# Performance work log

Measured on AMD Instinct MI355X. Metric: run time of the kernel, lower is better.

Reference implementation:

```python
import jax, jax.numpy as jnp
import numpy as np

D_MODEL = 1024
N_HEADS = 16
D_HEAD = 64


def setup_inputs() -> dict:
    key = jax.random.key(0)
    ks = jax.random.split(key, 9)
    B, T = 2, 2048
    s_in = 1.0 / np.sqrt(D_MODEL)
    s_o = 1.0 / np.sqrt(N_HEADS * D_HEAD)
    return {
        "x": jax.random.normal(ks[0], (B, T, D_MODEL), dtype=jnp.float32),
        "wq": jax.random.normal(ks[1], (D_MODEL, N_HEADS * D_HEAD), dtype=jnp.float32) * s_in,
        "bq": jax.random.normal(ks[2], (N_HEADS * D_HEAD,), dtype=jnp.float32) * 0.01,
        "wk": jax.random.normal(ks[3], (D_MODEL, N_HEADS * D_HEAD), dtype=jnp.float32) * s_in,
        "bk": jax.random.normal(ks[4], (N_HEADS * D_HEAD,), dtype=jnp.float32) * 0.01,
        "wv": jax.random.normal(ks[5], (D_MODEL, N_HEADS * D_HEAD), dtype=jnp.float32) * s_in,
        "bv": jax.random.normal(ks[6], (N_HEADS * D_HEAD,), dtype=jnp.float32) * 0.01,
        "wo": jax.random.normal(ks[7], (N_HEADS * D_HEAD, D_MODEL), dtype=jnp.float32) * s_o,
        "bo": jax.random.normal(ks[8], (D_MODEL,), dtype=jnp.float32) * 0.01,
    }


def reference(x, wq, bq, wk, bk, wv, bv, wo, bo):
    B, T, _ = x.shape
    H, Dh = N_HEADS, D_HEAD
    # projections -> [B, H, T, Dh]
    q = (x @ wq + bq).reshape(B, T, H, Dh).transpose(0, 2, 1, 3)
    k = (x @ wk + bk).reshape(B, T, H, Dh).transpose(0, 2, 1, 3)
    v = (x @ wv + bv).reshape(B, T, H, Dh).transpose(0, 2, 1, 3)
    scale = 1.0 / np.sqrt(Dh).astype(np.float32)
    attn = jnp.einsum("bhqd,bhkd->bhqk", q, k) * scale  # [B,H,T,T]
    causal = jnp.tril(jnp.ones((T, T), dtype=bool))
    attn = jnp.where(causal, attn, jnp.float32(-jnp.inf))
    attn = jax.nn.softmax(attn, axis=-1)
    out = jnp.einsum("bhqk,bhkd->bhqd", attn, v)  # [B,H,T,Dh]
    out = out.transpose(0, 2, 1, 3).reshape(B, T, H * Dh)
    return out @ wo + bo
```

## Files before the change

### kernel.cpp

```cpp
#include <hip/hip_runtime.h>
#include <math.h>

#define D_MODEL 1024
#define N_HEADS 16
#define D_HEAD  64
#define B_SZ    2
#define T_SEQ   2048
#define WN_ELEMS (1024u * 1024u)

typedef short bf16x8 __attribute__((ext_vector_type(8)));
typedef short bf16x4 __attribute__((ext_vector_type(4)));
typedef float f32x4  __attribute__((ext_vector_type(4)));
typedef unsigned short us4 __attribute__((ext_vector_type(4)));

__device__ __forceinline__ unsigned short f2bf(float f) {
  union { float f; unsigned u; } v; v.f = f;
  unsigned r = v.u + 0x7FFFu + ((v.u >> 16) & 1u);
  return (unsigned short)(r >> 16);
}
__device__ __forceinline__ float bf2f(unsigned short s) {
  union { unsigned u; float f; } v; v.u = ((unsigned)s) << 16;
  return v.f;
}
__device__ __forceinline__ unsigned pack2_rtz(float lo, float hi) {
  union { float f; unsigned u; } a, b; a.f = hi; b.f = lo;
  return __builtin_amdgcn_perm(a.u, b.u, 0x07060302u);
}

__device__ __forceinline__ void async_copy16(const unsigned short* g, unsigned short* l) {
  __builtin_amdgcn_global_load_lds(
      (__attribute__((address_space(1))) void*)(g),
      (__attribute__((address_space(3))) void*)(l), 16, 0, 0);
}

__device__ __forceinline__ size_t widx(int n, int k) {
  const int fb = n >> 5, mi = (n >> 4) & 1, lr = n & 15;
  const int kt = k >> 6, hf = (k >> 5) & 1, quad = (k >> 3) & 3, e = k & 7;
  return ((size_t)(fb * 16 + kt) * 4 + (mi * 2 + hf)) * 512 + (quad * 16 + lr) * 8 + e;
}

__device__ __forceinline__ unsigned short* opart_ptr(
    unsigned short* wtd, unsigned short* xbd, int p) {
  const size_t off = (size_t)p * 2048;
  const size_t RA  = (size_t)3 * 1024 * 1024;
  return (off < RA) ? (wtd + off) : (xbd + (off - RA));
}

__global__ __launch_bounds__(256) void conv_all(
    const float* __restrict__ x,
    const float* __restrict__ wq, const float* __restrict__ wk,
    const float* __restrict__ wv, const float* __restrict__ wo,
    unsigned short* __restrict__ wt, unsigned short* __restrict__ xb)
{
  const int z = blockIdx.z;
  if (z < 4) {
    const float* W = (z == 0) ? wq : (z == 1) ? wk : (z == 2) ? wv : wo;
    unsigned short* O = wt + (size_t)z * WN_ELEMS;
    __shared__ float t[32][33];
    const int tx = threadIdx.x & 31, ty = threadIdx.x >> 5;
    const int kb = blockIdx.x * 32, nb = blockIdx.y * 32;
    #pragma unroll
    for (int i = 0; i < 4; i++)
      t[ty + i * 8][tx] = W[(size_t)(kb + ty + i * 8) * D_MODEL + nb + tx];
    __syncthreads();
    #pragma unroll
    for (int i = 0; i < 4; i++)
      O[widx(nb + ty + i * 8, kb + tx)] = f2bf(t[tx][ty + i * 8]);
  } else {
    const int row = (z - 4) * 1024 + blockIdx.y * 32 + (threadIdx.x >> 3);
    const int col = blockIdx.x * 32 + (threadIdx.x & 7) * 4;
    float4 v = *(const float4*)&x[(size_t)row * D_MODEL + col];
    us4 o = { f2bf(v.x), f2bf(v.y), f2bf(v.z), f2bf(v.w) };
    *(us4*)&xb[(size_t)row * D_MODEL + col] = o;
  }
}

#define BKg 64
#define NTg (D_MODEL / BKg)
#define QSCALE 0.180336879f

__global__ __launch_bounds__(256) void qkv_gemm(
    const unsigned short* __restrict__ A, const unsigned short* __restrict__ Bt,
    const float* __restrict__ bq, const float* __restrict__ bk,
    const float* __restrict__ bv, unsigned short* __restrict__ qkv,
    unsigned short* __restrict__ vT)
{
  __shared__ unsigned short As[2][128 * BKg];

  const int tid  = threadIdx.x;
  const int wv   = tid >> 6;
  const int lane = tid & 63;
  const int lr   = lane & 15;
  const int quad = lane >> 4;
  const int wm   = wv >> 1;
  const int wn   = wv & 1;
  const int row0 = blockIdx.x * 128;
  const int col0 = blockIdx.y * 64;
  const int K = D_MODEL;

  const int mid = col0 >> 10;
  const float* bias = (mid == 0) ? bq : (mid == 1) ? bk : bv;

  f32x4 acc[8];
  #pragma unroll
  for (int i = 0; i < 8; i++) acc[i] = (f32x4){0.f, 0.f, 0.f, 0.f};

  auto stageA = [&](int buf, int k0) {
    #pragma unroll
    for (int it = 0; it < 4; it++) {
      const int gg = wv * 256 + it * 64 + lane;
      const int r  = gg >> 3;
      const int gc = ((gg & 7) ^ (r & 7)) * 8;
      async_copy16(A + (size_t)(row0 + r) * K + k0 + gc,
                   &As[buf][(size_t)(wv * 256 + it * 64) * 8]);
    }
  };

  const int wsel = (mid == 2) ? wn : wm;
  const int fb   = ((col0 & 1023) >> 5) + wsel;
  const unsigned short* Wp =
      Bt + (size_t)mid * WN_ELEMS + (size_t)fb * (16 * 2048) + lane * 8;

  auto loadW = [&](int kt, bf16x8 (&W)[2][2]) {
    #pragma unroll
    for (int mi = 0; mi < 2; mi++)
      #pragma unroll
      for (int hf = 0; hf < 2; hf++)
        W[mi][hf] = *(const bf16x8*)&Wp[((size_t)kt * 4 + mi * 2 + hf) * 512];
  };

  const int xrow = (mid == 2) ? wm : wn;

  bf16x8 Wc[2][2], Wn[2][2];
  loadW(0, Wc);
  stageA(0, 0);
  int cur = 0;

  auto kstep = [&](int t, bf16x8 (&Wuse)[2][2], bf16x8 (&Wpre)[2][2]) {
    __syncthreads();

    bf16x8 xF[4][2];
    #pragma unroll
    for (int hf = 0; hf < 2; hf++) {
      const int kc = ((hf * 4 + quad) ^ (lr & 7)) * 8;
      #pragma unroll
      for (int ni = 0; ni < 4; ni++)
        xF[ni][hf] = *(const bf16x8*)&As[cur][(xrow * 64 + ni * 16 + lr) * BKg + kc];
    }

    if (t + 1 < NTg) {
      stageA(cur ^ 1, (t + 1) * BKg);
      loadW(t + 1, Wpre);
    }

    if (mid == 2) {
      #pragma unroll
      for (int hf = 0; hf < 2; hf++)
        #pragma unroll
        for (int mi = 0; mi < 4; mi++)
          #pragma unroll
          for (int ni = 0; ni < 2; ni++)
            acc[mi * 2 + ni] = __builtin_amdgcn_mfma_f32_16x16x32_bf16(
                xF[mi][hf], Wuse[ni][hf], acc[mi * 2 + ni], 0, 0, 0);
    } else {
      #pragma unroll
      for (int hf = 0; hf < 2; hf++)
        #pragma unroll
        for (int mi = 0; mi < 2; mi++)
          #pragma unroll
          for (int ni = 0; ni < 4; ni++)
            acc[mi * 4 + ni] = __builtin_amdgcn_mfma_f32_16x16x32_bf16(
                Wuse[mi][hf], xF[ni][hf], acc[mi * 4 + ni], 0, 0, 0);
    }
    cur ^= 1;
  };

  #pragma unroll 1
  for (int t = 0; t < NTg; t += 2) {
    kstep(t,     Wc, Wn);
    kstep(t + 1, Wn, Wc);
  }

  if (mid == 2) {
    #pragma unroll
    for (int ni = 0; ni < 2; ni++) {
      const int nn = (col0 & 1023) + wn * 32 + ni * 16 + lr;
      const float bv_ = bias[nn];
      const int h = nn >> 6, d = nn & 63;
      #pragma unroll
      for (int mi = 0; mi < 4; mi++) {
        const int t0_ = row0 + wm * 64 + mi * 16 + quad * 4;
        const int b = t0_ >> 11, tl = t0_ & 2047;
        us4 o;
        #pragma unroll
        for (int i = 0; i < 4; i++) o[i] = f2bf(acc[mi * 2 + ni][i] + bv_);
        *(us4*)&vT[((size_t)(b * N_HEADS + h) * D_HEAD + d) * T_SEQ + tl] = o;
      }
    }
  } else {
    unsigned short* dst = qkv + (size_t)mid * (4096u * 1024u);
    const float qs = (mid == 0) ? QSCALE : 1.0f;
    #pragma unroll
    for (int ni = 0; ni < 4; ni++) {
      const int t = row0 + wn * 64 + ni * 16 + lr;
      const int b = t >> 11, tl = t & 2047;
      #pragma unroll
      for (int mi = 0; mi < 2; mi++) {
        const int f = (col0 & 1023) + wm * 32 + mi * 16 + quad * 4;
        const int h = f >> 6, d = f & 63;
        const float4 b4 = *(const float4*)&bias[f];
        us4 o;
        o[0] = f2bf((acc[mi * 4 + ni][0] + b4.x) * qs);
        o[1] = f2bf((acc[mi * 4 + ni][1] + b4.y) * qs);
        o[2] = f2bf((acc[mi * 4 + ni][2] + b4.z) * qs);
        o[3] = f2bf((acc[mi * 4 + ni][3] + b4.w) * qs);
        *(us4*)&dst[((size_t)(b * N_HEADS + h) * T_SEQ + tl) * D_HEAD + d] = o;
      }
    }
  }
}

__global__ __launch_bounds__(256) void mfma_gemm(
    const unsigned short* __restrict__ A, const unsigned short* __restrict__ Bt,
    const float* __restrict__ bias, float* __restrict__ C,
    int M, int N, int K)
{
  __shared__ unsigned short As[2][128 * BKg];

  const int tid  = threadIdx.x;
  const int wv   = tid >> 6;
  const int lane = tid & 63;
  const int lr   = lane & 15;
  const int quad = lane >> 4;
  const int wm   = wv >> 1;
  const int wn   = wv & 1;
  const int row0 = blockIdx.x * 128;
  const int col0 = blockIdx.y * 64;

  f32x4 acc[4][2];
  #pragma unroll
  for (int mi = 0; mi < 4; mi++)
    #pragma unroll
    for (int ni = 0; ni < 2; ni++) acc[mi][ni] = (f32x4){0.f, 0.f, 0.f, 0.f};

  auto stageA = [&](int buf, int k0) {
    #pragma unroll
    for (int it = 0; it < 4; it++) {
      const int gg = wv * 256 + it * 64 + lane;
      const int r  = gg >> 3;
      const int gc = ((gg & 7) ^ (r & 7)) * 8;
      async_copy16(A + (size_t)(row0 + r) * K + k0 + gc,
                   &As[buf][(size_t)(wv * 256 + it * 64) * 8]);
    }
  };

  const int fb = (col0 >> 5) + wn;
  const unsigned short* Wp = Bt + (size_t)fb * (16 * 2048) + lane * 8;
  auto loadW = [&](int kt, bf16x8 (&W)[2][2]) {
    #pragma unroll
    for (int ni = 0; ni < 2; ni++)
      #pragma unroll
      for (int hf = 0; hf < 2; hf++)
        W[ni][hf] = *(const bf16x8*)&Wp[((size_t)kt * 4 + ni * 2 + hf) * 512];
  };

  const int NT = K / BKg;
  bf16x8 Wc[2][2], Wn[2][2];
  loadW(0, Wc);
  stageA(0, 0);
  int cur = 0;

  auto kstep = [&](int t, bf16x8 (&Wuse)[2][2], bf16x8 (&Wpre)[2][2]) {
    __syncthreads();

    bf16x8 aF[4][2];
    #pragma unroll
    for (int hf = 0; hf < 2; hf++) {
      const int kc = ((hf * 4 + quad) ^ (lr & 7)) * 8;
      #pragma unroll
      for (int mi = 0; mi < 4; mi++)
        aF[mi][hf] = *(const bf16x8*)&As[cur][(wm * 64 + mi * 16 + lr) * BKg + kc];
    }

    if (t + 1 < NT) {
      stageA(cur ^ 1, (t + 1) * BKg);
      loadW(t + 1, Wpre);
    }

    #pragma unroll
    for (int hf = 0; hf < 2; hf++)
      #pragma unroll
      for (int mi = 0; mi < 4; mi++)
        #pragma unroll
        for (int ni = 0; ni < 2; ni++)
          acc[mi][ni] = __builtin_amdgcn_mfma_f32_16x16x32_bf16(
              aF[mi][hf], Wuse[ni][hf], acc[mi][ni], 0, 0, 0);
    cur ^= 1;
  };

  #pragma unroll 1
  for (int t = 0; t < NT; t += 2) {
    kstep(t,     Wc, Wn);
    kstep(t + 1, Wn, Wc);
  }

  #pragma unroll
  for (int ni = 0; ni < 2; ni++) {
    const int n = col0 + wn * 32 + ni * 16 + lr;
    const float bv = bias[n];
    #pragma unroll
    for (int mi = 0; mi < 4; mi++) {
      #pragma unroll
      for (int i = 0; i < 4; i++) {
        const int m = row0 + wm * 64 + mi * 16 + quad * 4 + i;
        C[(size_t)m * N + n] = acc[mi][ni][i] + bv;
      }
    }
  }
}

__global__ __launch_bounds__(256) void flash_part(
    const unsigned short* __restrict__ Q, const unsigned short* __restrict__ K,
    const unsigned short* __restrict__ Vt, unsigned short* __restrict__ Out,
    unsigned short* __restrict__ OpA, unsigned short* __restrict__ OpB,
    float* __restrict__ Lpart)
{
  const int bh = blockIdx.x;
  const int y  = blockIdx.y;
  int g, md;
  if (y < 28) { g = 15 - (y >> 1); md = 1 + (y & 1); }
  else        { g = 29 - y; md = 0; }

  const int b  = bh >> 4;
  const int h  = bh & 15;

  const unsigned short* Qb = Q  + (size_t)bh * T_SEQ * D_HEAD;
  const unsigned short* Kb = K  + (size_t)bh * T_SEQ * D_HEAD;
  const unsigned short* Vb = Vt + (size_t)bh * D_HEAD * T_SEQ;

  __shared__ __align__(16) unsigned short Ks[2][64 * 64];
  __shared__ __align__(16) unsigned short Vs[2][64 * 64];

  const int tid  = threadIdx.x;
  const int wv4  = tid >> 6;
  const int lane = tid & 63;
  const int lr   = lane & 15;
  const int quad = lane >> 4;

  const int qg      = 4 * g + wv4;
  const int q0      = qg * 32;
  const int my_full = 2 * g + 1 + (wv4 >> 1);
  const int tstart  = (md == 2) ? (g + 1) : 0;
  const int bend    = (md == 1) ? (g + 1) : (2 * g + 2);
  const int my_end  = (md == 1) ? (g + 1) : my_full;

  const int cbase = (tid & ~63);
  const int rr = tid >> 3;
  const int gcf = ((tid & 7) ^ (rr & 7)) * 8;
  const unsigned short* kp0 = Kb + (size_t)rr * D_HEAD + gcf;
  const unsigned short* vp0 = Vb + (size_t)rr * T_SEQ + gcf;

  auto stage = [&](int buf, int tile) {
    const unsigned short* kt = kp0 + (size_t)tile * (64 * D_HEAD);
    const unsigned short* vt = vp0 + (size_t)tile * 64;
    async_copy16(kt,                    &Ks[buf][(size_t)cbase * 8]);
    async_copy16(kt + 32 * D_HEAD,      &Ks[buf][(size_t)(256 + cbase) * 8]);
    async_copy16(vt,                    &Vs[buf][(size_t)cbase * 8]);
    async_copy16(vt + (size_t)32 * T_SEQ, &Vs[buf][(size_t)(256 + cbase) * 8]);
  };

  bf16x8 bQ[2][2];
  #pragma unroll
  for (int qb = 0; qb < 2; qb++)
    #pragma unroll
    for (int kh = 0; kh < 2; kh++)
      bQ[qb][kh] = *(const bf16x8*)&Qb[(size_t)(q0 + qb * 16 + lr) * D_HEAD + kh * 32 + quad * 8];

  f32x4 oacc[2][4];
  #pragma unroll
  for (int qb = 0; qb < 2; qb++)
    #pragma unroll
    for (int dt = 0; dt < 4; dt++) oacc[qb][dt] = (f32x4){0.f, 0.f, 0.f, 0.f};
  f32x4 lacc[2] = {(f32x4){0.f, 0.f, 0.f, 0.f}, (f32x4){0.f, 0.f, 0.f, 0.f}};

  const bf16x4 vONE = {(short)0x3F80, (short)0x3F80, (short)0x3F80, (short)0x3F80};

  int cur = 0;
  stage(0, tstart);

  for (int j = tstart; j < bend; j++) {
    __syncthreads();
    const bool act = (j < my_end);
    const unsigned short* KsB = &Ks[cur][0];
    const unsigned short* VsB = &Vs[cur][0];
    const int kv0 = j * 64;

    bf16x8 aK[4][2];
    bf16x4 aV[4][4];
    if (act) {
      #pragma unroll
      for (int nt = 0; nt < 4; nt++) {
        const int row = nt * 16 + lr;
        #pragma unroll
        for (int kh = 0; kh < 2; kh++) {
          const int sc = (kh * 4 + quad) ^ (row & 7);
          aK[nt][kh] = *(const bf16x8*)&KsB[row * 64 + sc * 8];
        }
      }
      #pragma unroll
      for (int dt = 0; dt < 4; dt++) {
        const int row = dt * 16 + lr;
        #pragma unroll
        for (int ks = 0; ks < 4; ks++) {
          const int sc = (ks * 2 + (quad >> 1)) ^ (row & 7);
          aV[dt][ks] = *(const bf16x4*)&VsB[row * 64 + sc * 8 + (quad & 1) * 4];
        }
      }
    }

    if (j + 1 < bend) stage(cur ^ 1, j + 1);

    if (act) {
      f32x4 sacc[2][4];
      __builtin_amdgcn_s_setprio(1);
      #pragma unroll
      for (int nt = 0; nt < 4; nt++) {
        #pragma unroll
        for (int qb = 0; qb < 2; qb++) {
          f32x4 c = (f32x4){0.f, 0.f, 0.f, 0.f};
          c = __builtin_amdgcn_mfma_f32_16x16x32_bf16(aK[nt][0], bQ[qb][0], c, 0, 0, 0);
          c = __builtin_amdgcn_mfma_f32_16x16x32_bf16(aK[nt][1], bQ[qb][1], c, 0, 0, 0);
          sacc[qb][nt] = c;
        }
      }
      __builtin_amdgcn_s_setprio(0);

      const bool diag = (j == my_full - 1);
      bf16x4 bP[2][4];
      #pragma unroll
      for (int qb = 0; qb < 2; qb++) {
        if (diag) {
          const int qcol = q0 + qb * 16 + lr;
          #pragma unroll
          for (int nt = 0; nt < 4; nt++)
            #pragma unroll
            for (int i = 0; i < 4; i++)
              if (kv0 + nt * 16 + quad * 4 + i > qcol) sacc[qb][nt][i] = -INFINITY;
        }
        #pragma unroll
        for (int nt = 0; nt < 4; nt++) {
          float p[4];
          #pragma unroll
          for (int i = 0; i < 4; i++)
            p[i] = __builtin_amdgcn_exp2f(sacc[qb][nt][i]);
          union { unsigned u[2]; bf16x4 v; } pk;
          pk.u[0] = pack2_rtz(p[0], p[1]);
          pk.u[1] = pack2_rtz(p[2], p[3]);
          bP[qb][nt] = pk.v;
        }
      }

      __builtin_amdgcn_s_setprio(1);
      #pragma unroll
      for (int ks = 0; ks < 4; ks++) {
        #pragma unroll
        for (int qb = 0; qb < 2; qb++) {
          lacc[qb] = __builtin_amdgcn_mfma_f32_16x16x16bf16_1k(
              vONE, bP[qb][ks], lacc[qb], 0, 0, 0);
          #pragma unroll
          for (int dt = 0; dt < 4; dt++)
            oacc[qb][dt] = __builtin_amdgcn_mfma_f32_16x16x16bf16_1k(
                aV[dt][ks], bP[qb][ks], oacc[qb][dt], 0, 0, 0);
        }
      }
      __builtin_amdgcn_s_setprio(0);
    }
    cur ^= 1;
  }

  float l_i[2] = {lacc[0][0], lacc[1][0]};

  if (md == 0) {
    #pragma unroll
    for (int qb = 0; qb < 2; qb++) {
      const float invl = __builtin_amdgcn_rcpf(l_i[qb]);
      const size_t orow = (size_t)(b * T_SEQ + q0 + qb * 16 + lr) * D_MODEL + h * D_HEAD;
      #pragma unroll
      for (int dt = 0; dt < 4; dt++) {
        us4 o;
        #pragma unroll
        for (int i = 0; i < 4; i++) o[i] = f2bf(oacc[qb][dt][i] * invl);
        *(us4*)&Out[orow + dt * 16 + quad * 4] = o;
      }
    }
  } else {
    const int s = md - 1;
    const int p = (bh * 56 + (qg - 8)) * 2 + s;
    unsigned short* Op = opart_ptr(OpA, OpB, p);
    if (quad == 0) {
      Lpart[(p * 2 + 0) * 16 + lr] = l_i[0];
      Lpart[(p * 2 + 1) * 16 + lr] = l_i[1];
    }
    #pragma unroll
    for (int qb = 0; qb < 2; qb++) {
      #pragma unroll
      for (int dt = 0; dt < 4; dt++) {
        us4 o;
        #pragma unroll
        for (int i = 0; i < 4; i++) o[i] = f2bf(oacc[qb][dt][i]);
        *(us4*)&Op[(size_t)(((qb * 4 + dt) * 64) + lane) * 4] = o;
      }
    }
  }
}

__global__ __launch_bounds__(64) void flash_reduce(
    unsigned short* __restrict__ OpA, unsigned short* __restrict__ OpB,
    const float* __restrict__ Lpart, unsigned short* __restrict__ Out)
{
  const int bh  = blockIdx.x;
  const int qgr = blockIdx.y;
  const int q0  = (8 + qgr) * 32;
  const int b   = bh >> 4;
  const int h   = bh & 15;
  const int lane = threadIdx.x;
  const int lr   = lane & 15;
  const int quad = lane >> 4;

  const int item = bh * 56 + qgr;
  const int p0 = item * 2, p1 = item * 2 + 1;
  const unsigned short* O0 = opart_ptr(OpA, OpB, p0);
  const unsigned short* O1 = opart_ptr(OpA, OpB, p1);

  #pragma unroll
  for (int qb = 0; qb < 2; qb++) {
    const float l0 = Lpart[(p0 * 2 + qb) * 16 + lr];
    const float l1 = Lpart[(p1 * 2 + qb) * 16 + lr];
    const float invL = __builtin_amdgcn_rcpf(l0 + l1);
    const size_t orow = (size_t)(b * T_SEQ + q0 + qb * 16 + lr) * D_MODEL + h * D_HEAD;
    #pragma unroll
    for (int dt = 0; dt < 4; dt++) {
      us4 o0 = *(const us4*)&O0[(size_t)(((qb * 4 + dt) * 64) + lane) * 4];
      us4 o1 = *(const us4*)&O1[(size_t)(((qb * 4 + dt) * 64) + lane) * 4];
      us4 o;
      #pragma unroll
      for (int i = 0; i < 4; i++)
        o[i] = f2bf((bf2f(o0[i]) + bf2f(o1[i])) * invL);
      *(us4*)&Out[orow + dt * 16 + quad * 4] = o;
    }
  }
}

extern "C" void kernel_launch(void* const* d_in, const int* in_sizes, int n_in,
                              void* d_out, int out_size, void* d_ws, size_t ws_size,
                              hipStream_t stream) {
  (void)in_sizes; (void)n_in; (void)out_size; (void)ws_size;

  const float* x  = (const float*)d_in[0];
  const float* wq = (const float*)d_in[1];
  const float* bq = (const float*)d_in[2];
  const float* wk = (const float*)d_in[3];
  const float* bk = (const float*)d_in[4];
  const float* wv = (const float*)d_in[5];
  const float* bv = (const float*)d_in[6];
  const float* wo = (const float*)d_in[7];
  const float* bo = (const float*)d_in[8];
  float* out = (float*)d_out;

  const int M = B_SZ * T_SEQ;
  const int N = D_MODEL;
  const int K = D_MODEL;
  const size_t MN = (size_t)M * N;
  const size_t WN = (size_t)N * N;

  unsigned short* wt    = (unsigned short*)d_ws;
  unsigned short* xb    = wt + 4 * WN;
  unsigned short* qkv   = xb + MN;
  unsigned short* qb    = qkv;
  unsigned short* kb    = qkv + MN;
  unsigned short* vT    = qkv + 2 * MN;
  unsigned short* attnb = vT + MN;
  float* Lpart = (float*)(attnb + MN);

  conv_all<<<dim3(32, 32, 8), dim3(256), 0, stream>>>(x, wq, wk, wv, wo, wt, xb);

  qkv_gemm<<<dim3(M / 128, 48), dim3(256), 0, stream>>>(xb, wt, bq, bk, bv, qkv, vT);

  flash_part<<<dim3(B_SZ * N_HEADS, 30), dim3(256), 0, stream>>>(
      qb, kb, vT, attnb, wt, xb, Lpart);
  flash_reduce<<<dim3(B_SZ * N_HEADS, 56), dim3(64), 0, stream>>>(
      wt, xb, Lpart, attnb);

  mfma_gemm<<<dim3(M / 128, N / 64), dim3(256), 0, stream>>>(attnb, wt + 3 * WN, bo, out, M, N, K);
}
```

Baseline: 188.9 us.

## Widen QKV GEMM tile to 128 columns, each wave spanning all rows

Each QKV GEMM block now computes 128 output columns instead of 64, with each of the four waves owning a 32-column strip across all 128 rows. This halves the number of blocks and the total re-staging of the activation tile into shared memory, while doubling accumulators per wave. The register double-buffered weight prefetch is removed, so weight loads are issued at the start of each k-step and their latency is no longer hidden behind the previous step's MFMAs. Register pressure rises, which may reduce occupancy.

```diff
diff --git a/kernel.cpp b/kernel.cpp
--- a/kernel.cpp
+++ b/kernel.cpp
@@ -92,18 +92,17 @@
   const int lane = tid & 63;
   const int lr   = lane & 15;
   const int quad = lane >> 4;
-  const int wm   = wv >> 1;
-  const int wn   = wv & 1;
   const int row0 = blockIdx.x * 128;
-  const int col0 = blockIdx.y * 64;
+  const int col0 = blockIdx.y * 128;
+  const int colL = col0 & 1023;
   const int K = D_MODEL;
 
   const int mid = col0 >> 10;
   const float* bias = (mid == 0) ? bq : (mid == 1) ? bk : bv;
 
-  f32x4 acc[8];
+  f32x4 acc[16];
   #pragma unroll
-  for (int i = 0; i < 8; i++) acc[i] = (f32x4){0.f, 0.f, 0.f, 0.f};
+  for (int i = 0; i < 16; i++) acc[i] = (f32x4){0.f, 0.f, 0.f, 0.f};
 
   auto stageA = [&](int buf, int k0) {
     #pragma unroll
@@ -116,80 +115,65 @@
     }
   };
 
-  const int wsel = (mid == 2) ? wn : wm;
-  const int fb   = ((col0 & 1023) >> 5) + wsel;
+  const int fb = (colL >> 5) + wv;
   const unsigned short* Wp =
       Bt + (size_t)mid * WN_ELEMS + (size_t)fb * (16 * 2048) + lane * 8;
 
-  auto loadW = [&](int kt, bf16x8 (&W)[2][2]) {
+  int cur = 0;
+  stageA(0, 0);
+
+  for (int t = 0; t < NTg; ++t) {
+    __syncthreads();
+
+    bf16x8 Wt[2][2];
     #pragma unroll
     for (int mi = 0; mi < 2; mi++)
       #pragma unroll
       for (int hf = 0; hf < 2; hf++)
-        W[mi][hf] = *(const bf16x8*)&Wp[((size_t)kt * 4 + mi * 2 + hf) * 512];
-  };
-
-  const int xrow = (mid == 2) ? wm : wn;
-
-  bf16x8 Wc[2][2], Wn[2][2];
-  loadW(0, Wc);
-  stageA(0, 0);
-  int cur = 0;
-
-  auto kstep = [&](int t, bf16x8 (&Wuse)[2][2], bf16x8 (&Wpre)[2][2]) {
-    __syncthreads();
-
-    bf16x8 xF[4][2];
+        Wt[mi][hf] = *(const bf16x8*)&Wp[((size_t)t * 4 + mi * 2 + hf) * 512];
+
+    bf16x8 xF[8][2];
     #pragma unroll
     for (int hf = 0; hf < 2; hf++) {
       const int kc = ((hf * 4 + quad) ^ (lr & 7)) * 8;
       #pragma unroll
-      for (int ni = 0; ni < 4; ni++)
-        xF[ni][hf] = *(const bf16x8*)&As[cur][(xrow * 64 + ni * 16 + lr) * BKg + kc];
-    }
-
-    if (t + 1 < NTg) {
-      stageA(cur ^ 1, (t + 1) * BKg);
-      loadW(t + 1, Wpre);
-    }
+      for (int nt = 0; nt < 8; nt++)
+        xF[nt][hf] = *(const bf16x8*)&As[cur][(nt * 16 + lr) * BKg + kc];
+    }
+
+    if (t + 1 < NTg) stageA(cur ^ 1, (t + 1) * BKg);
 
     if (mid == 2) {
       #pragma unroll
       for (int hf = 0; hf < 2; hf++)
         #pragma unroll
-        for (int mi = 0; mi < 4; mi++)
+        for (int mi = 0; mi < 8; mi++)
           #pragma unroll
           for (int ni = 0; ni < 2; ni++)
             acc[mi * 2 + ni] = __builtin_amdgcn_mfma_f32_16x16x32_bf16(
-                xF[mi][hf], Wuse[ni][hf], acc[mi * 2 + ni], 0, 0, 0);
+                xF[mi][hf], Wt[ni][hf], acc[mi * 2 + ni], 0, 0, 0);
     } else {
       #pragma unroll
       for (int hf = 0; hf < 2; hf++)
         #pragma unroll
         for (int mi = 0; mi < 2; mi++)
           #pragma unroll
-          for (int ni = 0; ni < 4; ni++)
-            acc[mi * 4 + ni] = __builtin_amdgcn_mfma_f32_16x16x32_bf16(
-                Wuse[mi][hf], xF[ni][hf], acc[mi * 4 + ni], 0, 0, 0);
+          for (int ni = 0; ni < 8; ni++)
+            acc[mi * 8 + ni] = __builtin_amdgcn_mfma_f32_16x16x32_bf16(
+                Wt[mi][hf], xF[ni][hf], acc[mi * 8 + ni], 0, 0, 0);
     }
     cur ^= 1;
-  };
-
-  #pragma unroll 1
-  for (int t = 0; t < NTg; t += 2) {
-    kstep(t,     Wc, Wn);
-    kstep(t + 1, Wn, Wc);
   }
 
   if (mid == 2) {
     #pragma unroll
     for (int ni = 0; ni < 2; ni++) {
-      const int nn = (col0 & 1023) + wn * 32 + ni * 16 + lr;
+      const int nn = colL + wv * 32 + ni * 16 + lr;
       const float bv_ = bias[nn];
       const int h = nn >> 6, d = nn & 63;
       #pragma unroll
-      for (int mi = 0; mi < 4; mi++) {
-        const int t0_ = row0 + wm * 64 + mi * 16 + quad * 4;
+      for (int mi = 0; mi < 8; mi++) {
+        const int t0_ = row0 + mi * 16 + quad * 4;
         const int b = t0_ >> 11, tl = t0_ & 2047;
         us4 o;
         #pragma unroll
@@ -201,19 +185,19 @@
     unsigned short* dst = qkv + (size_t)mid * (4096u * 1024u);
     const float qs = (mid == 0) ? QSCALE : 1.0f;
     #pragma unroll
-    for (int ni = 0; ni < 4; ni++) {
-      const int t = row0 + wn * 64 + ni * 16 + lr;
+    for (int ni = 0; ni < 8; ni++) {
+      const int t = row0 + ni * 16 + lr;
       const int b = t >> 11, tl = t & 2047;
       #pragma unroll
       for (int mi = 0; mi < 2; mi++) {
-        const int f = (col0 & 1023) + wm * 32 + mi * 16 + quad * 4;
+        const int f = colL + wv * 32 + mi * 16 + quad * 4;
         const int h = f >> 6, d = f & 63;
         const float4 b4 = *(const float4*)&bias[f];
         us4 o;
-        o[0] = f2bf((acc[mi * 4 + ni][0] + b4.x) * qs);
-        o[1] = f2bf((acc[mi * 4 + ni][1] + b4.y) * qs);
-        o[2] = f2bf((acc[mi * 4 + ni][2] + b4.z) * qs);
-        o[3] = f2bf((acc[mi * 4 + ni][3] + b4.w) * qs);
+        o[0] = f2bf((acc[mi * 8 + ni][0] + b4.x) * qs);
+        o[1] = f2bf((acc[mi * 8 + ni][1] + b4.y) * qs);
+        o[2] = f2bf((acc[mi * 8 + ni][2] + b4.z) * qs);
+        o[3] = f2bf((acc[mi * 8 + ni][3] + b4.w) * qs);
         *(us4*)&dst[((size_t)(b * N_HEADS + h) * T_SEQ + tl) * D_HEAD + d] = o;
       }
     }
@@ -584,7 +568,7 @@
 
   conv_all<<<dim3(32, 32, 8), dim3(256), 0, stream>>>(x, wq, wk, wv, wo, wt, xb);
 
-  qkv_gemm<<<dim3(M / 128, 48), dim3(256), 0, stream>>>(xb, wt, bq, bk, bv, qkv, vT);
+  qkv_gemm<<<dim3(M / 128, 24), dim3(256), 0, stream>>>(xb, wt, bq, bk, bv, qkv, vT);
 
   flash_part<<<dim3(B_SZ * N_HEADS, 30), dim3(256), 0, stream>>>(
       qb, kb, vT, attnb, wt, xb, Lpart);
```

After: 200.8 us. 6.4% more time.
